# Optimization experiments

Hardware: AMD Instinct MI355X
Metric: run time of the kernel (lower is better)

## Reference

```python
import jax, jax.numpy as jnp
import numpy as np

MODEL_DIM = 1024
NUM_HEADS = 16
HEAD_DIM = MODEL_DIM // NUM_HEADS
B, S = 4, 2048


def setup_inputs() -> dict:
    key = jax.random.key(0)
    ks = jax.random.split(key, 12)
    sc = 1.0 / np.sqrt(MODEL_DIM)
    inp = {
        'query': jax.random.normal(ks[0], (B, S, MODEL_DIM), jnp.float32),
        'key': jax.random.normal(ks[1], (B, S, MODEL_DIM), jnp.float32),
        'value': jax.random.normal(ks[2], (B, S, MODEL_DIM), jnp.float32),
        # causal mask, 1 = attend, 0 = blocked
        'mask': jnp.tril(jnp.ones((S, S), jnp.int32))[None, None],
        'wq': jax.random.normal(ks[3], (MODEL_DIM, MODEL_DIM), jnp.float32) * sc,
        'bq': jax.random.normal(ks[4], (MODEL_DIM,), jnp.float32) * sc,
        'wk': jax.random.normal(ks[5], (MODEL_DIM, MODEL_DIM), jnp.float32) * sc,
        'bk': jax.random.normal(ks[6], (MODEL_DIM,), jnp.float32) * sc,
        'wv': jax.random.normal(ks[7], (MODEL_DIM, MODEL_DIM), jnp.float32) * sc,
        'bv': jax.random.normal(ks[8], (MODEL_DIM,), jnp.float32) * sc,
        'wo': jax.random.normal(ks[9], (MODEL_DIM, MODEL_DIM), jnp.float32) * sc,
        'bo': jax.random.normal(ks[10], (MODEL_DIM,), jnp.float32) * sc,
    }
    return inp


def reference(query, key, value, mask, wq, bq, wk, bk, wv, bv, wo, bo):
    # projections: x @ W^T + b  (torch Linear convention)
    Q = query @ wq.T + bq
    K = key @ wk.T + bk
    V = value @ wv.T + bv
    # [B, S, D] -> [B, H, S, hd]
    def split_heads(x):
        return x.reshape(B, -1, NUM_HEADS, HEAD_DIM).transpose(0, 2, 1, 3)
    Qh, Kh, Vh = split_heads(Q), split_heads(K), split_heads(V)
    energy = jnp.einsum('bhqd,bhkd->bhqk', Qh, Kh) / jnp.sqrt(jnp.float32(HEAD_DIM))
    energy = jnp.where(mask == 0, jnp.float32(-1e10), energy)
    attn = jax.nn.softmax(energy, axis=-1)
    x = jnp.einsum('bhqk,bhkd->bhqd', attn, Vh)
    x = x.transpose(0, 2, 1, 3).reshape(B, -1, MODEL_DIM)
    return x @ wo.T + bo  # dropout is identity in eval / p=0
```

## Files before the change

### kernel.cpp

```cpp
#include <hip/hip_runtime.h>
#include <hip/hip_bf16.h>
#include <cstdint>

#define MODEL_DIM 1024
#define NUM_HEADS 16
#define HEAD_DIM 64
#define BATCH 4
#define SEQ 2048
#define M_TOT (BATCH * SEQ)
#define KSTEP 64
#define QSCALE 0.1803368801111729f

typedef float f32x4 __attribute__((ext_vector_type(4)));
typedef unsigned short ushort8 __attribute__((ext_vector_type(8)));
typedef unsigned short ushort4v __attribute__((ext_vector_type(4)));
typedef __bf16 bf16x8 __attribute__((ext_vector_type(8)));

union BF8 { ushort8 u; bf16x8 b; ushort4v h4[2]; };

__device__ inline unsigned short f2bf(float f) {
  union { float f; unsigned int u; } x;
  x.f = f;
  unsigned int u = x.u;
  u += 0x7fffu + ((u >> 16) & 1u);
  return (unsigned short)(u >> 16);
}

__device__ __forceinline__ float e2(float x) {
  return __builtin_amdgcn_exp2f(x);
}

__device__ inline f32x4 mfma16(bf16x8 a, bf16x8 b, f32x4 c) {
  return __builtin_amdgcn_mfma_f32_16x16x32_bf16(a, b, c, 0, 0, 0);
}

__device__ __forceinline__ void gload_lds16(const void* g, void* l) {
  __builtin_amdgcn_global_load_lds(
      (const __attribute__((address_space(1))) unsigned int*)g,
      (__attribute__((address_space(3))) unsigned int*)l, 16, 0, 0);
}

__global__ __launch_bounds__(256) void convert_w_kernel(
    const float* __restrict__ w0, const float* __restrict__ w1,
    const float* __restrict__ w2, unsigned short* __restrict__ o0,
    unsigned short* __restrict__ o1, unsigned short* __restrict__ o2) {
  const int gid = blockIdx.x * 256 + threadIdx.x;
  const int tsel = gid >> 17;
  const size_t off = (size_t)(gid & 131071) * 8;
  const float* s = tsel == 0 ? w0 : tsel == 1 ? w1 : w2;
  unsigned short* d = tsel == 0 ? o0 : tsel == 1 ? o1 : o2;
  float4 a = ((const float4*)(s + off))[0];
  float4 b = ((const float4*)(s + off))[1];
  ushort8 u;
  u[0] = f2bf(a.x); u[1] = f2bf(a.y); u[2] = f2bf(a.z); u[3] = f2bf(a.w);
  u[4] = f2bf(b.x); u[5] = f2bf(b.y); u[6] = f2bf(b.z); u[7] = f2bf(b.w);
  *(ushort8*)(d + off) = u;
}

__global__ __launch_bounds__(256) void convert_w1_kernel(
    const float* __restrict__ s, unsigned short* __restrict__ d) {
  const int gid = blockIdx.x * 256 + threadIdx.x;
  const size_t off = (size_t)gid * 8;
  float4 a = ((const float4*)(s + off))[0];
  float4 b = ((const float4*)(s + off))[1];
  ushort8 u;
  u[0] = f2bf(a.x); u[1] = f2bf(a.y); u[2] = f2bf(a.z); u[3] = f2bf(a.w);
  u[4] = f2bf(b.x); u[5] = f2bf(b.y); u[6] = f2bf(b.z); u[7] = f2bf(b.w);
  *(ushort8*)(d + off) = u;
}

template <bool ABF16, bool WBF16, int OUT_MODE>
__global__ __launch_bounds__(256) void gemm_kernel(
    const void* __restrict__ Ap, const void* __restrict__ Wp,
    const float* __restrict__ bias, void* __restrict__ Cp, float oscale) {
  constexpr int K = MODEL_DIM;
  constexpr int ABYTES = ABF16 ? 8192 : 16384;
  constexpr int WBYTES = WBF16 ? 8192 : 16384;
  const int bid = blockIdx.x;
  const int wg = (bid & 7) * 64 + (bid >> 3);
  const int m0 = (wg >> 3) * 128;
  const int n0 = (wg & 7) * 128;

  __shared__ __align__(16) unsigned char smem[2 * (ABYTES + WBYTES)];

  const int tid = threadIdx.x;
  const int lane = tid & 63, wid = tid >> 6;
  const int l15 = lane & 15, lg = lane >> 4;
  const int wm = wid >> 1, wn = wid & 1;

  auto stage = [&](int buf, int k0) {
    unsigned char* ab = smem + buf * (ABYTES + WBYTES);
    unsigned char* bb = ab + ABYTES;
    if (ABF16) {
      const unsigned short* A = (const unsigned short*)Ap;
#pragma unroll
      for (int s = 0; s < 2; ++s) {
        const int row = s * 64 + wid * 16 + (lane >> 2);
        gload_lds16(A + (size_t)(m0 + row) * K + k0 + (lane & 3) * 8,
                    ab + (s * 64 + wid * 16) * 64);
      }
    } else {
      const float* A = (const float*)Ap;
#pragma unroll
      for (int s = 0; s < 4; ++s) {
        const int row = s * 32 + wid * 8 + (lane >> 3);
        gload_lds16(A + (size_t)(m0 + row) * K + k0 + (lane & 7) * 4,
                    ab + (s * 32 + wid * 8) * 128);
      }
    }
    if (WBF16) {
      const unsigned short* W = (const unsigned short*)Wp;
#pragma unroll
      for (int s = 0; s < 2; ++s) {
        const int row = s * 64 + wid * 16 + (lane >> 2);
        gload_lds16(W + (size_t)(n0 + row) * K + k0 + (lane & 3) * 8,
                    bb + (s * 64 + wid * 16) * 64);
      }
    } else {
      const float* W = (const float*)Wp;
#pragma unroll
      for (int s = 0; s < 4; ++s) {
        const int row = s * 32 + wid * 8 + (lane >> 3);
        gload_lds16(W + (size_t)(n0 + row) * K + k0 + (lane & 7) * 4,
                    bb + (s * 32 + wid * 8) * 128);
      }
    }
  };

  f32x4 acc[4][4];
#pragma unroll
  for (int i = 0; i < 4; ++i)
#pragma unroll
    for (int j = 0; j < 4; ++j) acc[i][j] = (f32x4){0.f, 0.f, 0.f, 0.f};

  stage(0, 0);
  __syncthreads();
  int cur = 0;
  for (int t = 0; t < K / 32; ++t) {
    if (t + 1 < K / 32) stage(cur ^ 1, (t + 1) * 32);
    unsigned char* ab = smem + cur * (ABYTES + WBYTES);
    unsigned char* bb = ab + ABYTES;
    BF8 af[4], bf[4];
#pragma unroll
    for (int tt = 0; tt < 4; ++tt) {
      const int arow = wm * 64 + tt * 16 + l15;
      if (ABF16) {
        af[tt].u = *(const ushort8*)(ab + arow * 64 + lg * 16);
      } else {
        const float* ar = (const float*)(ab + arow * 128 + lg * 32);
        f32x4 a0 = *(const f32x4*)ar;
        f32x4 a1 = *(const f32x4*)(ar + 4);
#pragma unroll
        for (int jj = 0; jj < 4; ++jj) {
          af[tt].b[jj] = (__bf16)a0[jj];
          af[tt].b[4 + jj] = (__bf16)a1[jj];
        }
      }
      const int brow = wn * 64 + tt * 16 + l15;
      if (WBF16) {
        bf[tt].u = *(const ushort8*)(bb + brow * 64 + lg * 16);
      } else {
        const float* br = (const float*)(bb + brow * 128 + lg * 32);
        f32x4 b0 = *(const f32x4*)br;
        f32x4 b1 = *(const f32x4*)(br + 4);
#pragma unroll
        for (int jj = 0; jj < 4; ++jj) {
          bf[tt].b[jj] = (__bf16)b0[jj];
          bf[tt].b[4 + jj] = (__bf16)b1[jj];
        }
      }
    }
#pragma unroll
    for (int mt = 0; mt < 4; ++mt)
#pragma unroll
      for (int nt = 0; nt < 4; ++nt)
        acc[mt][nt] = mfma16(af[mt].b, bf[nt].b, acc[mt][nt]);
    __syncthreads();
    cur ^= 1;
  }

#pragma unroll
  for (int nt = 0; nt < 4; ++nt) {
    const int col = n0 + wn * 64 + nt * 16 + l15;
    const float bv = bias[col];
#pragma unroll
    for (int mt = 0; mt < 4; ++mt) {
      const int rowb = m0 + wm * 64 + mt * 16 + lg * 4;
      if (OUT_MODE == 2) {
        ushort4v w;
#pragma unroll
        for (int i = 0; i < 4; ++i) w[i] = f2bf((acc[mt][nt][i] + bv) * oscale);
        *(ushort4v*)((unsigned short*)Cp + (size_t)col * M_TOT + rowb) = w;
      } else {
#pragma unroll
        for (int i = 0; i < 4; ++i) {
          const float v = (acc[mt][nt][i] + bv) * oscale;
          if (OUT_MODE == 1)
            ((unsigned short*)Cp)[(size_t)(rowb + i) * MODEL_DIM + col] = f2bf(v);
          else
            ((float*)Cp)[(size_t)(rowb + i) * MODEL_DIM + col] = v;
        }
      }
    }
  }
}

__device__ __forceinline__ void qk_sm(
    int k0, int r0, int l15, int lg, const BF8 (&kf)[4][2], const BF8 (&qf)[2][2],
    float (&li)[2], BF8 (&pf)[2][2]) {
  const f32x4 zero = {0.f, 0.f, 0.f, 0.f};
  f32x4 stT[4][2];
#pragma unroll
  for (int kt = 0; kt < 4; ++kt)
#pragma unroll
    for (int qs = 0; qs < 2; ++qs) {
      f32x4 a = mfma16(kf[kt][0].b, qf[qs][0].b, zero);
      stT[kt][qs] = mfma16(kf[kt][1].b, qf[qs][1].b, a);
    }
  const bool mm = (k0 + KSTEP > r0);
#pragma unroll
  for (int qs = 0; qs < 2; ++qs) {
    float p[4][4];
#pragma unroll
    for (int kt = 0; kt < 4; ++kt)
#pragma unroll
      for (int i = 0; i < 4; ++i)
        p[kt][i] = e2(stT[kt][qs][i]);
    if (mm) {
#pragma unroll
      for (int kt = 0; kt < 4; ++kt)
#pragma unroll
        for (int i = 0; i < 4; ++i) {
          const int ktok = k0 + kt * 16 + lg * 4 + i;
          const int q = r0 + qs * 16 + l15;
          if (ktok > q) p[kt][i] = 0.f;
        }
    }
    float rs = 0.f;
#pragma unroll
    for (int kt = 0; kt < 4; ++kt)
#pragma unroll
      for (int i = 0; i < 4; ++i) rs += p[kt][i];
    rs += __shfl_xor(rs, 16);
    rs += __shfl_xor(rs, 32);
    li[qs] += rs;
#pragma unroll
    for (int ks = 0; ks < 2; ++ks)
#pragma unroll
      for (int i = 0; i < 4; ++i) {
        pf[qs][ks].b[i] = (__bf16)p[ks * 2][i];
        pf[qs][ks].b[4 + i] = (__bf16)p[ks * 2 + 1][i];
      }
  }
}

__global__ __launch_bounds__(256) void attn_kernel(
    const unsigned short* __restrict__ Qb, const unsigned short* __restrict__ Kb,
    const unsigned short* __restrict__ Vt, unsigned short* __restrict__ Ctx) {
  const int bx = blockIdx.x;
  const int bh = bx & 63;
  const int tile = 15 - (bx >> 6);
  const int b = bh >> 4, h = bh & 15;
  const int tid = threadIdx.x;
  const int lane = tid & 63, wid = tid >> 6;
  const int l15 = lane & 15, lg = lane >> 4;
  const size_t tokb = (size_t)b * SEQ;
  const int r0 = tile * 128 + wid * 32;
  const int nsteps = (tile + 1) * 2;

  __shared__ unsigned short lds[2][128 * 64];

  const int srow8 = lane >> 3;
  const int sgr = (lane & 7) ^ srow8;

  auto stage = [&](int buf, int k0) {
#pragma unroll
    for (int i = 0; i < 2; ++i) {
      const int row = wid * 16 + i * 8 + srow8;
      gload_lds16(Kb + (tokb + k0 + row) * MODEL_DIM + h * HEAD_DIM + sgr * 8,
                  &lds[buf][(wid * 16 + i * 8) * 64]);
    }
#pragma unroll
    for (int i = 0; i < 2; ++i) {
      const int dim = wid * 16 + i * 8 + srow8;
      gload_lds16(Vt + (size_t)(h * HEAD_DIM + dim) * M_TOT + tokb + k0 + sgr * 8,
                  &lds[buf][(64 + wid * 16 + i * 8) * 64]);
    }
  };

  BF8 qf[2][2];
#pragma unroll
  for (int qs = 0; qs < 2; ++qs) {
    const unsigned short* qp =
        Qb + (tokb + r0 + qs * 16 + l15) * MODEL_DIM + h * HEAD_DIM + lg * 8;
    qf[qs][0].u = *(const ushort8*)qp;
    qf[qs][1].u = *(const ushort8*)(qp + 32);
  }

  float li[2] = {0.f, 0.f};
  f32x4 o[4][2];
#pragma unroll
  for (int ds = 0; ds < 4; ++ds)
#pragma unroll
    for (int qs = 0; qs < 2; ++qs) o[ds][qs] = (f32x4){0.f, 0.f, 0.f, 0.f};

  stage(0, 0);
  __syncthreads();

  int cur = 0;
  for (int t = 0; t < nsteps; ++t) {
    const int k0 = t * KSTEP;
    if (t + 1 < nsteps) stage(cur ^ 1, (t + 1) * KSTEP);

    const bool act = k0 < r0 + 32;

    BF8 kf[4][2];
#pragma unroll
    for (int kt = 0; kt < 4; ++kt)
#pragma unroll
      for (int half = 0; half < 2; ++half) {
        const int row = kt * 16 + l15;
        const int idx = row * 64 + (((lg + half * 4) ^ (l15 & 7)) * 8);
        kf[kt][half].u = *(const ushort8*)(&lds[cur][idx]);
      }

    BF8 pf[2][2];
    if (act) qk_sm(k0, r0, l15, lg, kf, qf, li, pf);

#pragma unroll
    for (int ks = 0; ks < 2; ++ks) {
      BF8 vf[4];
#pragma unroll
      for (int ds = 0; ds < 4; ++ds) {
        const int row = 64 + ds * 16 + l15;
        const int g0 = (ks * 4 + (lg >> 1)) ^ (l15 & 7);
        const int g1 = (ks * 4 + 2 + (lg >> 1)) ^ (l15 & 7);
        const int so = (lg & 1) * 4;
        vf[ds].h4[0] = *(const ushort4v*)(&lds[cur][row * 64 + g0 * 8 + so]);
        vf[ds].h4[1] = *(const ushort4v*)(&lds[cur][row * 64 + g1 * 8 + so]);
      }
      if (act) {
#pragma unroll
        for (int ds = 0; ds < 4; ++ds)
#pragma unroll
          for (int qs = 0; qs < 2; ++qs)
            o[ds][qs] = mfma16(vf[ds].b, pf[qs][ks].b, o[ds][qs]);
      }
    }
    __syncthreads();
    cur ^= 1;
  }

#pragma unroll
  for (int qs = 0; qs < 2; ++qs) {
    const float inv = 1.0f / li[qs];
    const size_t rowc = (tokb + r0 + qs * 16 + l15) * MODEL_DIM + h * HEAD_DIM;
#pragma unroll
    for (int ds = 0; ds < 4; ++ds) {
      ushort4v w;
#pragma unroll
      for (int i = 0; i < 4; ++i) w[i] = f2bf(o[ds][qs][i] * inv);
      *(ushort4v*)(&Ctx[rowc + ds * 16 + lg * 4]) = w;
    }
  }
}

extern "C" void kernel_launch(void* const* d_in, const int* in_sizes, int n_in,
                              void* d_out, int out_size, void* d_ws, size_t ws_size,
                              hipStream_t stream) {
  (void)in_sizes; (void)n_in; (void)out_size; (void)ws_size;
  const float* query = (const float*)d_in[0];
  const float* key = (const float*)d_in[1];
  const float* value = (const float*)d_in[2];
  const float* wq = (const float*)d_in[4];
  const float* bq = (const float*)d_in[5];
  const float* wk = (const float*)d_in[6];
  const float* bk = (const float*)d_in[7];
  const float* wv = (const float*)d_in[8];
  const float* bv = (const float*)d_in[9];
  const float* wo = (const float*)d_in[10];
  const float* bo = (const float*)d_in[11];

  const size_t NM = (size_t)M_TOT * MODEL_DIM;
  const size_t NW = (size_t)MODEL_DIM * MODEL_DIM;
  unsigned short* Qb = (unsigned short*)d_ws;
  unsigned short* Kb = Qb + NM;
  unsigned short* Vt = Kb + NM;
  unsigned short* Ctx = Qb;
  unsigned short* wob = Kb;
  unsigned short* wqb = (unsigned short*)d_out;
  unsigned short* wkb = wqb + NW;
  unsigned short* wvb = wkb + NW;

  convert_w_kernel<<<dim3(1536), dim3(256), 0, stream>>>(wq, wk, wv, wqb, wkb, wvb);

  const dim3 gg(512), gb(256);
  gemm_kernel<false, true, 1><<<gg, gb, 0, stream>>>(query, wqb, bq, Qb, QSCALE);
  gemm_kernel<false, true, 1><<<gg, gb, 0, stream>>>(key, wkb, bk, Kb, 1.0f);
  gemm_kernel<false, true, 2><<<gg, gb, 0, stream>>>(value, wvb, bv, Vt, 1.0f);

  attn_kernel<<<dim3(1024), gb, 0, stream>>>(Qb, Kb, Vt, Ctx);

  convert_w1_kernel<<<dim3(512), gb, 0, stream>>>(wo, wob);

  gemm_kernel<true, true, 0><<<gg, gb, 0, stream>>>(Ctx, wob, bo, (float*)d_out, 1.0f);
}
```

Baseline: 185.6 us.

## Merge Q/K/V projections into one launch and halve attention query tile

The three separate projection GEMM launches become a single 1536-block kernel that picks the input, weight, bias and output layout per block group, removing launch gaps and tail effects between the GEMMs. The attention kernel now processes 64 query rows per block (16 per wave) instead of 128, doubling the grid to 2048 blocks for better load balance across the causal triangle. In exchange each K/V tile loaded into LDS is reused by half as many queries, raising total K/V staging traffic, and the fused GEMM duplicates the GEMM code.

```diff
diff --git a/kernel.cpp b/kernel.cpp
--- a/kernel.cpp
+++ b/kernel.cpp
@@ -69,6 +69,112 @@
   *(ushort8*)(d + off) = u;
 }
 
+__global__ __launch_bounds__(256) void qkv_gemm_kernel(
+    const float* __restrict__ query, const float* __restrict__ key,
+    const float* __restrict__ value, const unsigned short* __restrict__ wqb,
+    const unsigned short* __restrict__ wkb, const unsigned short* __restrict__ wvb,
+    const float* __restrict__ bq, const float* __restrict__ bk,
+    const float* __restrict__ bv, unsigned short* __restrict__ Qb,
+    unsigned short* __restrict__ Kb, unsigned short* __restrict__ Vt) {
+  constexpr int K = MODEL_DIM;
+  constexpr int ABYTES = 16384;
+  constexpr int WBYTES = 8192;
+  const int bid = blockIdx.x;
+  const int grp = bid >> 9;
+  const int bin = bid & 511;
+  const float* A = grp == 0 ? query : grp == 1 ? key : value;
+  const unsigned short* W = grp == 0 ? wqb : grp == 1 ? wkb : wvb;
+  const float* bias = grp == 0 ? bq : grp == 1 ? bk : bv;
+  const float oscale = grp == 0 ? QSCALE : 1.0f;
+  const int wg = (bin & 7) * 64 + (bin >> 3);
+  const int m0 = (wg >> 3) * 128;
+  const int n0 = (wg & 7) * 128;
+
+  __shared__ __align__(16) unsigned char smem[2 * (ABYTES + WBYTES)];
+
+  const int tid = threadIdx.x;
+  const int lane = tid & 63, wid = tid >> 6;
+  const int l15 = lane & 15, lg = lane >> 4;
+  const int wm = wid >> 1, wn = wid & 1;
+
+  auto stage = [&](int buf, int k0) {
+    unsigned char* ab = smem + buf * (ABYTES + WBYTES);
+    unsigned char* bb = ab + ABYTES;
+#pragma unroll
+    for (int s = 0; s < 4; ++s) {
+      const int row = s * 32 + wid * 8 + (lane >> 3);
+      gload_lds16(A + (size_t)(m0 + row) * K + k0 + (lane & 7) * 4,
+                  ab + (s * 32 + wid * 8) * 128);
+    }
+#pragma unroll
+    for (int s = 0; s < 2; ++s) {
+      const int row = s * 64 + wid * 16 + (lane >> 2);
+      gload_lds16(W + (size_t)(n0 + row) * K + k0 + (lane & 3) * 8,
+                  bb + (s * 64 + wid * 16) * 64);
+    }
+  };
+
+  f32x4 acc[4][4];
+#pragma unroll
+  for (int i = 0; i < 4; ++i)
+#pragma unroll
+    for (int j = 0; j < 4; ++j) acc[i][j] = (f32x4){0.f, 0.f, 0.f, 0.f};
+
+  stage(0, 0);
+  __syncthreads();
+  int cur = 0;
+  for (int t = 0; t < K / 32; ++t) {
+    if (t + 1 < K / 32) stage(cur ^ 1, (t + 1) * 32);
+    unsigned char* ab = smem + cur * (ABYTES + WBYTES);
+    unsigned char* bb = ab + ABYTES;
+    BF8 af[4], bf[4];
+#pragma unroll
+    for (int tt = 0; tt < 4; ++tt) {
+      const int arow = wm * 64 + tt * 16 + l15;
+      const float* ar = (const float*)(ab + arow * 128 + lg * 32);
+      f32x4 a0 = *(const f32x4*)ar;
+      f32x4 a1 = *(const f32x4*)(ar + 4);
+#pragma unroll
+      for (int jj = 0; jj < 4; ++jj) {
+        af[tt].b[jj] = (__bf16)a0[jj];
+        af[tt].b[4 + jj] = (__bf16)a1[jj];
+      }
+      const int brow = wn * 64 + tt * 16 + l15;
+      bf[tt].u = *(const ushort8*)(bb + brow * 64 + lg * 16);
+    }
+#pragma unroll
+    for (int mt = 0; mt < 4; ++mt)
+#pragma unroll
+      for (int nt = 0; nt < 4; ++nt)
+        acc[mt][nt] = mfma16(af[mt].b, bf[nt].b, acc[mt][nt]);
+    __syncthreads();
+    cur ^= 1;
+  }
+
+  unsigned short* Crm = grp == 0 ? Qb : Kb;
+#pragma unroll
+  for (int nt = 0; nt < 4; ++nt) {
+    const int col = n0 + wn * 64 + nt * 16 + l15;
+    const float bv_ = bias[col];
+#pragma unroll
+    for (int mt = 0; mt < 4; ++mt) {
+      const int rowb = m0 + wm * 64 + mt * 16 + lg * 4;
+      if (grp == 2) {
+        ushort4v w;
+#pragma unroll
+        for (int i = 0; i < 4; ++i) w[i] = f2bf(acc[mt][nt][i] + bv_);
+        *(ushort4v*)(Vt + (size_t)col * M_TOT + rowb) = w;
+      } else {
+#pragma unroll
+        for (int i = 0; i < 4; ++i) {
+          const float v = (acc[mt][nt][i] + bv_) * oscale;
+          Crm[(size_t)(rowb + i) * MODEL_DIM + col] = f2bf(v);
+        }
+      }
+    }
+  }
+}
+
 template <bool ABF16, bool WBF16, int OUT_MODE>
 __global__ __launch_bounds__(256) void gemm_kernel(
     const void* __restrict__ Ap, const void* __restrict__ Wp,
@@ -206,52 +312,46 @@
 }
 
 __device__ __forceinline__ void qk_sm(
-    int k0, int r0, int l15, int lg, const BF8 (&kf)[4][2], const BF8 (&qf)[2][2],
-    float (&li)[2], BF8 (&pf)[2][2]) {
+    int k0, int r0, int l15, int lg, const BF8 (&kf)[4][2], const BF8 (&qf)[2],
+    float& li, BF8 (&pf)[2]) {
   const f32x4 zero = {0.f, 0.f, 0.f, 0.f};
-  f32x4 stT[4][2];
+  f32x4 stT[4];
+#pragma unroll
+  for (int kt = 0; kt < 4; ++kt) {
+    f32x4 a = mfma16(kf[kt][0].b, qf[0].b, zero);
+    stT[kt] = mfma16(kf[kt][1].b, qf[1].b, a);
+  }
+  const bool mm = (k0 + KSTEP > r0);
+  float p[4][4];
 #pragma unroll
   for (int kt = 0; kt < 4; ++kt)
 #pragma unroll
-    for (int qs = 0; qs < 2; ++qs) {
-      f32x4 a = mfma16(kf[kt][0].b, qf[qs][0].b, zero);
-      stT[kt][qs] = mfma16(kf[kt][1].b, qf[qs][1].b, a);
-    }
-  const bool mm = (k0 + KSTEP > r0);
-#pragma unroll
-  for (int qs = 0; qs < 2; ++qs) {
-    float p[4][4];
+    for (int i = 0; i < 4; ++i)
+      p[kt][i] = e2(stT[kt][i]);
+  if (mm) {
 #pragma unroll
     for (int kt = 0; kt < 4; ++kt)
 #pragma unroll
-      for (int i = 0; i < 4; ++i)
-        p[kt][i] = e2(stT[kt][qs][i]);
-    if (mm) {
-#pragma unroll
-      for (int kt = 0; kt < 4; ++kt)
-#pragma unroll
-        for (int i = 0; i < 4; ++i) {
-          const int ktok = k0 + kt * 16 + lg * 4 + i;
-          const int q = r0 + qs * 16 + l15;
-          if (ktok > q) p[kt][i] = 0.f;
-        }
-    }
-    float rs = 0.f;
-#pragma unroll
-    for (int kt = 0; kt < 4; ++kt)
-#pragma unroll
-      for (int i = 0; i < 4; ++i) rs += p[kt][i];
-    rs += __shfl_xor(rs, 16);
-    rs += __shfl_xor(rs, 32);
-    li[qs] += rs;
-#pragma unroll
-    for (int ks = 0; ks < 2; ++ks)
-#pragma unroll
       for (int i = 0; i < 4; ++i) {
-        pf[qs][ks].b[i] = (__bf16)p[ks * 2][i];
-        pf[qs][ks].b[4 + i] = (__bf16)p[ks * 2 + 1][i];
-      }
-  }
+        const int ktok = k0 + kt * 16 + lg * 4 + i;
+        if (ktok > r0 + l15) p[kt][i] = 0.f;
+      }
+  }
+  float rs = 0.f;
+#pragma unroll
+  for (int kt = 0; kt < 4; ++kt)
+#pragma unroll
+    for (int i = 0; i < 4; ++i) rs += p[kt][i];
+  rs += __shfl_xor(rs, 16);
+  rs += __shfl_xor(rs, 32);
+  li += rs;
+#pragma unroll
+  for (int ks = 0; ks < 2; ++ks)
+#pragma unroll
+    for (int i = 0; i < 4; ++i) {
+      pf[ks].b[i] = (__bf16)p[ks * 2][i];
+      pf[ks].b[4 + i] = (__bf16)p[ks * 2 + 1][i];
+    }
 }
 
 __global__ __launch_bounds__(256) void attn_kernel(
@@ -259,14 +359,14 @@
     const unsigned short* __restrict__ Vt, unsigned short* __restrict__ Ctx) {
   const int bx = blockIdx.x;
   const int bh = bx & 63;
-  const int tile = 15 - (bx >> 6);
+  const int tile = 31 - (bx >> 6);
   const int b = bh >> 4, h = bh & 15;
   const int tid = threadIdx.x;
   const int lane = tid & 63, wid = tid >> 6;
   const int l15 = lane & 15, lg = lane >> 4;
   const size_t tokb = (size_t)b * SEQ;
-  const int r0 = tile * 128 + wid * 32;
-  const int nsteps = (tile + 1) * 2;
+  const int r0 = tile * 64 + wid * 16;
+  const int nsteps = tile + 1;
 
   __shared__ unsigned short lds[2][128 * 64];
 
@@ -288,21 +388,18 @@
     }
   };
 
-  BF8 qf[2][2];
-#pragma unroll
-  for (int qs = 0; qs < 2; ++qs) {
+  BF8 qf[2];
+  {
     const unsigned short* qp =
-        Qb + (tokb + r0 + qs * 16 + l15) * MODEL_DIM + h * HEAD_DIM + lg * 8;
-    qf[qs][0].u = *(const ushort8*)qp;
-    qf[qs][1].u = *(const ushort8*)(qp + 32);
-  }
-
-  float li[2] = {0.f, 0.f};
-  f32x4 o[4][2];
-#pragma unroll
-  for (int ds = 0; ds < 4; ++ds)
-#pragma unroll
-    for (int qs = 0; qs < 2; ++qs) o[ds][qs] = (f32x4){0.f, 0.f, 0.f, 0.f};
+        Qb + (tokb + r0 + l15) * MODEL_DIM + h * HEAD_DIM + lg * 8;
+    qf[0].u = *(const ushort8*)qp;
+    qf[1].u = *(const ushort8*)(qp + 32);
+  }
+
+  float li = 0.f;
+  f32x4 o[4];
+#pragma unroll
+  for (int ds = 0; ds < 4; ++ds) o[ds] = (f32x4){0.f, 0.f, 0.f, 0.f};
 
   stage(0, 0);
   __syncthreads();
@@ -312,7 +409,7 @@
     const int k0 = t * KSTEP;
     if (t + 1 < nsteps) stage(cur ^ 1, (t + 1) * KSTEP);
 
-    const bool act = k0 < r0 + 32;
+    const bool act = k0 < r0 + 16;
 
     BF8 kf[4][2];
 #pragma unroll
@@ -324,7 +421,7 @@
         kf[kt][half].u = *(const ushort8*)(&lds[cur][idx]);
       }
 
-    BF8 pf[2][2];
+    BF8 pf[2];
     if (act) qk_sm(k0, r0, l15, lg, kf, qf, li, pf);
 
 #pragma unroll
@@ -342,24 +439,21 @@
       if (act) {
 #pragma unroll
         for (int ds = 0; ds < 4; ++ds)
-#pragma unroll
-          for (int qs = 0; qs < 2; ++qs)
-            o[ds][qs] = mfma16(vf[ds].b, pf[qs][ks].b, o[ds][qs]);
+          o[ds] = mfma16(vf[ds].b, pf[ks].b, o[ds]);
       }
     }
     __syncthreads();
     cur ^= 1;
   }
 
-#pragma unroll
-  for (int qs = 0; qs < 2; ++qs) {
-    const float inv = 1.0f / li[qs];
-    const size_t rowc = (tokb + r0 + qs * 16 + l15) * MODEL_DIM + h * HEAD_DIM;
+  {
+    const float inv = 1.0f / li;
+    const size_t rowc = (tokb + r0 + l15) * MODEL_DIM + h * HEAD_DIM;
 #pragma unroll
     for (int ds = 0; ds < 4; ++ds) {
       ushort4v w;
 #pragma unroll
-      for (int i = 0; i < 4; ++i) w[i] = f2bf(o[ds][qs][i] * inv);
+      for (int i = 0; i < 4; ++i) w[i] = f2bf(o[ds][i] * inv);
       *(ushort4v*)(&Ctx[rowc + ds * 16 + lg * 4]) = w;
     }
   }
@@ -394,14 +488,13 @@
 
   convert_w_kernel<<<dim3(1536), dim3(256), 0, stream>>>(wq, wk, wv, wqb, wkb, wvb);
 
-  const dim3 gg(512), gb(256);
-  gemm_kernel<false, true, 1><<<gg, gb, 0, stream>>>(query, wqb, bq, Qb, QSCALE);
-  gemm_kernel<false, true, 1><<<gg, gb, 0, stream>>>(key, wkb, bk, Kb, 1.0f);
-  gemm_kernel<false, true, 2><<<gg, gb, 0, stream>>>(value, wvb, bv, Vt, 1.0f);
-
-  attn_kernel<<<dim3(1024), gb, 0, stream>>>(Qb, Kb, Vt, Ctx);
-
-  convert_w1_kernel<<<dim3(512), gb, 0, stream>>>(wo, wob);
-
-  gemm_kernel<true, true, 0><<<gg, gb, 0, stream>>>(Ctx, wob, bo, (float*)d_out, 1.0f);
-}
+  qkv_gemm_kernel<<<dim3(1536), dim3(256), 0, stream>>>(
+      query, key, value, wqb, wkb, wvb, bq, bk, bv, Qb, Kb, Vt);
+
+  attn_kernel<<<dim3(2048), dim3(256), 0, stream>>>(Qb, Kb, Vt, Ctx);
+
+  convert_w1_kernel<<<dim3(512), dim3(256), 0, stream>>>(wo, wob);
+
+  gemm_kernel<true, true, 0><<<dim3(512), dim3(256), 0, stream>>>(
+      Ctx, wob, bo, (float*)d_out, 1.0f);
+}
```

Result: slower. 199.2 us (+7.3%).

## Swizzle GEMM LDS tiles and halve attention query tile to 64 rows

Applied to the files above, without the earlier changes.

The GEMM staging and fragment reads now XOR-swizzle the 16-byte column groups in LDS, which is meant to cut bank conflicts on the row-strided fragment loads. The attention kernel now gives each wave 16 query rows instead of 32, so a block covers 64 queries and the grid doubles to 2048 blocks. This gives finer causal load balance and more parallelism, but each staged K/V tile is reused by half as many queries, so K/V traffic per query rises.

```diff
diff --git a/kernel.cpp b/kernel.cpp
--- a/kernel.cpp
+++ b/kernel.cpp
@@ -88,6 +88,9 @@
   const int l15 = lane & 15, lg = lane >> 4;
   const int wm = wid >> 1, wn = wid & 1;
 
+  const int sg8 = (lane & 7) ^ (lane >> 3);
+  const int sg4 = (lane & 3) ^ ((lane >> 3) & 3);
+
   auto stage = [&](int buf, int k0) {
     unsigned char* ab = smem + buf * (ABYTES + WBYTES);
     unsigned char* bb = ab + ABYTES;
@@ -96,7 +99,7 @@
 #pragma unroll
       for (int s = 0; s < 2; ++s) {
         const int row = s * 64 + wid * 16 + (lane >> 2);
-        gload_lds16(A + (size_t)(m0 + row) * K + k0 + (lane & 3) * 8,
+        gload_lds16(A + (size_t)(m0 + row) * K + k0 + sg4 * 8,
                     ab + (s * 64 + wid * 16) * 64);
       }
     } else {
@@ -104,7 +107,7 @@
 #pragma unroll
       for (int s = 0; s < 4; ++s) {
         const int row = s * 32 + wid * 8 + (lane >> 3);
-        gload_lds16(A + (size_t)(m0 + row) * K + k0 + (lane & 7) * 4,
+        gload_lds16(A + (size_t)(m0 + row) * K + k0 + sg8 * 4,
                     ab + (s * 32 + wid * 8) * 128);
       }
     }
@@ -113,7 +116,7 @@
 #pragma unroll
       for (int s = 0; s < 2; ++s) {
         const int row = s * 64 + wid * 16 + (lane >> 2);
-        gload_lds16(W + (size_t)(n0 + row) * K + k0 + (lane & 3) * 8,
+        gload_lds16(W + (size_t)(n0 + row) * K + k0 + sg4 * 8,
                     bb + (s * 64 + wid * 16) * 64);
       }
     } else {
@@ -121,7 +124,7 @@
 #pragma unroll
       for (int s = 0; s < 4; ++s) {
         const int row = s * 32 + wid * 8 + (lane >> 3);
-        gload_lds16(W + (size_t)(n0 + row) * K + k0 + (lane & 7) * 4,
+        gload_lds16(W + (size_t)(n0 + row) * K + k0 + sg8 * 4,
                     bb + (s * 32 + wid * 8) * 128);
       }
     }
@@ -145,11 +148,14 @@
     for (int tt = 0; tt < 4; ++tt) {
       const int arow = wm * 64 + tt * 16 + l15;
       if (ABF16) {
-        af[tt].u = *(const ushort8*)(ab + arow * 64 + lg * 16);
+        const int g = lg ^ ((arow >> 1) & 3);
+        af[tt].u = *(const ushort8*)(ab + arow * 64 + g * 16);
       } else {
-        const float* ar = (const float*)(ab + arow * 128 + lg * 32);
-        f32x4 a0 = *(const f32x4*)ar;
-        f32x4 a1 = *(const f32x4*)(ar + 4);
+        const unsigned char* arp = ab + arow * 128;
+        const int g0 = (2 * lg) ^ (arow & 7);
+        const int g1 = (2 * lg + 1) ^ (arow & 7);
+        f32x4 a0 = *(const f32x4*)(arp + g0 * 16);
+        f32x4 a1 = *(const f32x4*)(arp + g1 * 16);
 #pragma unroll
         for (int jj = 0; jj < 4; ++jj) {
           af[tt].b[jj] = (__bf16)a0[jj];
@@ -158,11 +164,14 @@
       }
       const int brow = wn * 64 + tt * 16 + l15;
       if (WBF16) {
-        bf[tt].u = *(const ushort8*)(bb + brow * 64 + lg * 16);
+        const int g = lg ^ ((brow >> 1) & 3);
+        bf[tt].u = *(const ushort8*)(bb + brow * 64 + g * 16);
       } else {
-        const float* br = (const float*)(bb + brow * 128 + lg * 32);
-        f32x4 b0 = *(const f32x4*)br;
-        f32x4 b1 = *(const f32x4*)(br + 4);
+        const unsigned char* brp = bb + brow * 128;
+        const int g0 = (2 * lg) ^ (brow & 7);
+        const int g1 = (2 * lg + 1) ^ (brow & 7);
+        f32x4 b0 = *(const f32x4*)(brp + g0 * 16);
+        f32x4 b1 = *(const f32x4*)(brp + g1 * 16);
 #pragma unroll
         for (int jj = 0; jj < 4; ++jj) {
           bf[tt].b[jj] = (__bf16)b0[jj];
@@ -206,52 +215,46 @@
 }
 
 __device__ __forceinline__ void qk_sm(
-    int k0, int r0, int l15, int lg, const BF8 (&kf)[4][2], const BF8 (&qf)[2][2],
-    float (&li)[2], BF8 (&pf)[2][2]) {
+    int k0, int r0, int l15, int lg, const BF8 (&kf)[4][2], const BF8 (&qf)[2],
+    float& li, BF8 (&pf)[2]) {
   const f32x4 zero = {0.f, 0.f, 0.f, 0.f};
-  f32x4 stT[4][2];
+  f32x4 stT[4];
+#pragma unroll
+  for (int kt = 0; kt < 4; ++kt) {
+    f32x4 a = mfma16(kf[kt][0].b, qf[0].b, zero);
+    stT[kt] = mfma16(kf[kt][1].b, qf[1].b, a);
+  }
+  const bool mm = (k0 + KSTEP > r0);
+  float p[4][4];
 #pragma unroll
   for (int kt = 0; kt < 4; ++kt)
 #pragma unroll
-    for (int qs = 0; qs < 2; ++qs) {
-      f32x4 a = mfma16(kf[kt][0].b, qf[qs][0].b, zero);
-      stT[kt][qs] = mfma16(kf[kt][1].b, qf[qs][1].b, a);
-    }
-  const bool mm = (k0 + KSTEP > r0);
-#pragma unroll
-  for (int qs = 0; qs < 2; ++qs) {
-    float p[4][4];
+    for (int i = 0; i < 4; ++i)
+      p[kt][i] = e2(stT[kt][i]);
+  if (mm) {
 #pragma unroll
     for (int kt = 0; kt < 4; ++kt)
 #pragma unroll
-      for (int i = 0; i < 4; ++i)
-        p[kt][i] = e2(stT[kt][qs][i]);
-    if (mm) {
-#pragma unroll
-      for (int kt = 0; kt < 4; ++kt)
-#pragma unroll
-        for (int i = 0; i < 4; ++i) {
-          const int ktok = k0 + kt * 16 + lg * 4 + i;
-          const int q = r0 + qs * 16 + l15;
-          if (ktok > q) p[kt][i] = 0.f;
-        }
-    }
-    float rs = 0.f;
-#pragma unroll
-    for (int kt = 0; kt < 4; ++kt)
-#pragma unroll
-      for (int i = 0; i < 4; ++i) rs += p[kt][i];
-    rs += __shfl_xor(rs, 16);
-    rs += __shfl_xor(rs, 32);
-    li[qs] += rs;
-#pragma unroll
-    for (int ks = 0; ks < 2; ++ks)
-#pragma unroll
       for (int i = 0; i < 4; ++i) {
-        pf[qs][ks].b[i] = (__bf16)p[ks * 2][i];
-        pf[qs][ks].b[4 + i] = (__bf16)p[ks * 2 + 1][i];
-      }
-  }
+        const int ktok = k0 + kt * 16 + lg * 4 + i;
+        if (ktok > r0 + l15) p[kt][i] = 0.f;
+      }
+  }
+  float rs = 0.f;
+#pragma unroll
+  for (int kt = 0; kt < 4; ++kt)
+#pragma unroll
+    for (int i = 0; i < 4; ++i) rs += p[kt][i];
+  rs += __shfl_xor(rs, 16);
+  rs += __shfl_xor(rs, 32);
+  li += rs;
+#pragma unroll
+  for (int ks = 0; ks < 2; ++ks)
+#pragma unroll
+    for (int i = 0; i < 4; ++i) {
+      pf[ks].b[i] = (__bf16)p[ks * 2][i];
+      pf[ks].b[4 + i] = (__bf16)p[ks * 2 + 1][i];
+    }
 }
 
 __global__ __launch_bounds__(256) void attn_kernel(
@@ -259,14 +262,14 @@
     const unsigned short* __restrict__ Vt, unsigned short* __restrict__ Ctx) {
   const int bx = blockIdx.x;
   const int bh = bx & 63;
-  const int tile = 15 - (bx >> 6);
+  const int tile = 31 - (bx >> 6);
   const int b = bh >> 4, h = bh & 15;
   const int tid = threadIdx.x;
   const int lane = tid & 63, wid = tid >> 6;
   const int l15 = lane & 15, lg = lane >> 4;
   const size_t tokb = (size_t)b * SEQ;
-  const int r0 = tile * 128 + wid * 32;
-  const int nsteps = (tile + 1) * 2;
+  const int r0 = tile * 64 + wid * 16;
+  const int nsteps = tile + 1;
 
   __shared__ unsigned short lds[2][128 * 64];
 
@@ -288,21 +291,18 @@
     }
   };
 
-  BF8 qf[2][2];
-#pragma unroll
-  for (int qs = 0; qs < 2; ++qs) {
+  BF8 qf[2];
+  {
     const unsigned short* qp =
-        Qb + (tokb + r0 + qs * 16 + l15) * MODEL_DIM + h * HEAD_DIM + lg * 8;
-    qf[qs][0].u = *(const ushort8*)qp;
-    qf[qs][1].u = *(const ushort8*)(qp + 32);
-  }
-
-  float li[2] = {0.f, 0.f};
-  f32x4 o[4][2];
-#pragma unroll
-  for (int ds = 0; ds < 4; ++ds)
-#pragma unroll
-    for (int qs = 0; qs < 2; ++qs) o[ds][qs] = (f32x4){0.f, 0.f, 0.f, 0.f};
+        Qb + (tokb + r0 + l15) * MODEL_DIM + h * HEAD_DIM + lg * 8;
+    qf[0].u = *(const ushort8*)qp;
+    qf[1].u = *(const ushort8*)(qp + 32);
+  }
+
+  float li = 0.f;
+  f32x4 o[4];
+#pragma unroll
+  for (int ds = 0; ds < 4; ++ds) o[ds] = (f32x4){0.f, 0.f, 0.f, 0.f};
 
   stage(0, 0);
   __syncthreads();
@@ -312,7 +312,7 @@
     const int k0 = t * KSTEP;
     if (t + 1 < nsteps) stage(cur ^ 1, (t + 1) * KSTEP);
 
-    const bool act = k0 < r0 + 32;
+    const bool act = k0 < r0 + 16;
 
     BF8 kf[4][2];
 #pragma unroll
@@ -324,7 +324,7 @@
         kf[kt][half].u = *(const ushort8*)(&lds[cur][idx]);
       }
 
-    BF8 pf[2][2];
+    BF8 pf[2];
     if (act) qk_sm(k0, r0, l15, lg, kf, qf, li, pf);
 
 #pragma unroll
@@ -342,24 +342,21 @@
       if (act) {
 #pragma unroll
         for (int ds = 0; ds < 4; ++ds)
-#pragma unroll
-          for (int qs = 0; qs < 2; ++qs)
-            o[ds][qs] = mfma16(vf[ds].b, pf[qs][ks].b, o[ds][qs]);
+          o[ds] = mfma16(vf[ds].b, pf[ks].b, o[ds]);
       }
     }
     __syncthreads();
     cur ^= 1;
   }
 
-#pragma unroll
-  for (int qs = 0; qs < 2; ++qs) {
-    const float inv = 1.0f / li[qs];
-    const size_t rowc = (tokb + r0 + qs * 16 + l15) * MODEL_DIM + h * HEAD_DIM;
+  {
+    const float inv = 1.0f / li;
+    const size_t rowc = (tokb + r0 + l15) * MODEL_DIM + h * HEAD_DIM;
 #pragma unroll
     for (int ds = 0; ds < 4; ++ds) {
       ushort4v w;
 #pragma unroll
-      for (int i = 0; i < 4; ++i) w[i] = f2bf(o[ds][qs][i] * inv);
+      for (int i = 0; i < 4; ++i) w[i] = f2bf(o[ds][i] * inv);
       *(ushort4v*)(&Ctx[rowc + ds * 16 + lg * 4]) = w;
     }
   }
@@ -399,7 +396,7 @@
   gemm_kernel<false, true, 1><<<gg, gb, 0, stream>>>(key, wkb, bk, Kb, 1.0f);
   gemm_kernel<false, true, 2><<<gg, gb, 0, stream>>>(value, wvb, bv, Vt, 1.0f);
 
-  attn_kernel<<<dim3(1024), gb, 0, stream>>>(Qb, Kb, Vt, Ctx);
+  attn_kernel<<<dim3(2048), gb, 0, stream>>>(Qb, Kb, Vt, Ctx);
 
   convert_w1_kernel<<<dim3(512), gb, 0, stream>>>(wo, wob);
 
```

After: 209.0 us. +12.6%, slower.
